# Performance work log

Hardware: AMD Instinct MI355X
Metric: run time of the kernel (lower is better)

## Reference

```python
import jax, jax.numpy as jnp
import numpy as np

N = 50000      # nodes
E = 800000     # edges
IN = 128       # in_channels
H = 128        # hidden_channels
OUT = 40       # out_channels (classes)
EPS = 1e-5     # LayerNorm eps


def _glorot(key, fan_in, fan_out):
    lim = np.sqrt(6.0 / (fan_in + fan_out)).astype(np.float32)
    return jax.random.uniform(key, (fan_in, fan_out), jnp.float32, -lim, lim)


def setup_inputs() -> dict:
    key = jax.random.key(0)
    ks = jax.random.split(key, 8)
    x = jax.random.normal(ks[0], (N, IN), jnp.float32)
    edge_index = jax.random.randint(ks[1], (2, E), 0, N, jnp.int32)
    return {
        "x": x,
        "W0": _glorot(ks[2], IN, H), "b0": jnp.zeros((H,), jnp.float32),
        "W1": _glorot(ks[3], H, H),  "b1": jnp.zeros((H,), jnp.float32),
        "W2": _glorot(ks[4], H, OUT), "b2": jnp.zeros((OUT,), jnp.float32),
        "ln1_g": jnp.ones((H,), jnp.float32), "ln1_b": jnp.zeros((H,), jnp.float32),
        "ln2_g": jnp.ones((H,), jnp.float32), "ln2_b": jnp.zeros((H,), jnp.float32),
        "edge_index": edge_index,
    }


def reference(x, W0, b0, W1, b1, W2, b2, ln1_g, ln1_b, ln2_g, ln2_b, edge_index):
    # GCN normalization with self-loops: A_hat = D^-1/2 (A + I) D^-1/2
    self_idx = jnp.arange(N, dtype=edge_index.dtype)
    src = jnp.concatenate([edge_index[0], self_idx])  # [E+N]
    dst = jnp.concatenate([edge_index[1], self_idx])
    deg = jax.ops.segment_sum(jnp.ones_like(src, jnp.float32), dst, num_segments=N)
    dinv = jax.lax.rsqrt(deg)  # deg >= 1 thanks to self-loops
    norm = dinv[src] * dinv[dst]  # [E+N]

    def conv(h, W, b):
        h = h @ W                                  # [N, F] dense GEMM
        msg = h[src] * norm[:, None]               # gather + scale [E+N, F]
        return jax.ops.segment_sum(msg, dst, num_segments=N) + b

    def layernorm(h, g, b):
        mu = jnp.mean(h, axis=-1, keepdims=True)
        var = jnp.mean(jnp.square(h - mu), axis=-1, keepdims=True)
        return (h - mu) * jax.lax.rsqrt(var + EPS) * g + b

    # layer 0 (note: original uses lns[i+1], so lns[0] is never applied)
    h = jax.nn.relu(layernorm(conv(x, W0, b0), ln1_g, ln1_b))
    # dropout is identity in eval mode
    h = jax.nn.relu(layernorm(conv(h, W1, b1), ln2_g, ln2_b))
    h = conv(h, W2, b2)
    return jax.nn.log_softmax(h, axis=-1)
```

## Files before the change

### kernel.cpp

```cpp
#include <hip/hip_runtime.h>
#include <math.h>

typedef __attribute__((ext_vector_type(8))) short bf16x8;
typedef __attribute__((ext_vector_type(4))) float f32x4;
typedef unsigned short u16;
typedef unsigned int u32;

static __device__ __forceinline__ u16 f2bf(float f) {
    unsigned u = __float_as_uint(f);
    unsigned r = (u + 0x7fff + ((u >> 16) & 1)) >> 16;
    return (u16)r;
}
static __device__ __forceinline__ float bf2f(u16 h) {
    return __uint_as_float(((unsigned)h) << 16);
}
static __device__ __forceinline__ float pk_lo(u32 u) { return __uint_as_float(u << 16); }
static __device__ __forceinline__ float pk_hi(u32 u) { return __uint_as_float(u & 0xffff0000u); }

__global__ void init_k(int* __restrict__ counts, int n, int gN,
                       const float* __restrict__ W0, const float* __restrict__ W1,
                       const float* __restrict__ W2,
                       u16* __restrict__ w0hi, u16* __restrict__ w0lo,
                       u16* __restrict__ w1hi, u16* __restrict__ w1lo,
                       u16* __restrict__ w2hi, u16* __restrict__ w2lo) {
    int b = blockIdx.x;
    if (b < gN) {
        int i = b * 256 + threadIdx.x;
        if (i < n) counts[i] = 0;
        return;
    }
    int i = (b - gN) * 256 + threadIdx.x;
    const float* W; u16 *hi, *lo; int COLS, cin, idx;
    if (i < 16384)      { W = W0; hi = w0hi; lo = w0lo; COLS = 128; cin = 128; idx = i; }
    else if (i < 32768) { W = W1; hi = w1hi; lo = w1lo; COLS = 128; cin = 128; idx = i - 16384; }
    else if (i < 40960) { W = W2; hi = w2hi; lo = w2lo; COLS = 64;  cin = 40;  idx = i - 32768; }
    else return;
    int k = idx / COLS, col = idx % COLS;
    float v = (col < cin) ? W[k * cin + col] : 0.f;
    u16 h = f2bf(v);
    u16 l = f2bf(v - bf2f(h));
    int ct = col >> 4, ks = k >> 5, ln = (col & 15) + (((k >> 3) & 3) << 4), j = k & 7;
    int pos = (((ct * 4 + ks) * 64 + ln) << 3) + j;
    hi[pos] = h; lo[pos] = l;
}

static __device__ __forceinline__ void gemm1_body(int bid, const float* __restrict__ A,
                                                  const u16* __restrict__ Whi,
                                                  const u16* __restrict__ Wlo,
                                                  u16* __restrict__ C, int nrows) {
    constexpr int COLS = 128;
    int wave = threadIdx.x >> 6, lane = threadIdx.x & 63;
    int r0 = bid * 64 + wave * 16;
    int arow = min(r0 + (lane & 15), nrows - 1);
    int kbase = (lane >> 4) * 8;

    bf16x8 ahi[4], alo[4];
#pragma unroll
    for (int ks = 0; ks < 4; ++ks) {
        const float* ap = &A[(long)arow * 128 + ks * 32 + kbase];
        float4 f0 = *(const float4*)ap;
        float4 f1 = *(const float4*)(ap + 4);
        float fv[8] = {f0.x, f0.y, f0.z, f0.w, f1.x, f1.y, f1.z, f1.w};
#pragma unroll
        for (int j = 0; j < 8; ++j) {
            u16 h = f2bf(fv[j]);
            ahi[ks][j] = (short)h;
            alo[ks][j] = (short)f2bf(fv[j] - bf2f(h));
        }
    }
#pragma unroll
    for (int ct = 0; ct < COLS / 16; ct += 2) {
        f32x4 acc0 = {0.f, 0.f, 0.f, 0.f}, acc1 = {0.f, 0.f, 0.f, 0.f};
#pragma unroll
        for (int ks = 0; ks < 4; ++ks) {
            int fo0 = ((ct * 4 + ks) * 64 + lane) * 8;
            int fo1 = (((ct + 1) * 4 + ks) * 64 + lane) * 8;
            bf16x8 bhi0 = *(const bf16x8*)&Whi[fo0];
            bf16x8 blo0 = *(const bf16x8*)&Wlo[fo0];
            bf16x8 bhi1 = *(const bf16x8*)&Whi[fo1];
            bf16x8 blo1 = *(const bf16x8*)&Wlo[fo1];
            acc0 = __builtin_amdgcn_mfma_f32_16x16x32_bf16(ahi[ks], bhi0, acc0, 0, 0, 0);
            acc1 = __builtin_amdgcn_mfma_f32_16x16x32_bf16(ahi[ks], bhi1, acc1, 0, 0, 0);
            acc0 = __builtin_amdgcn_mfma_f32_16x16x32_bf16(alo[ks], bhi0, acc0, 0, 0, 0);
            acc1 = __builtin_amdgcn_mfma_f32_16x16x32_bf16(alo[ks], bhi1, acc1, 0, 0, 0);
            acc0 = __builtin_amdgcn_mfma_f32_16x16x32_bf16(ahi[ks], blo0, acc0, 0, 0, 0);
            acc1 = __builtin_amdgcn_mfma_f32_16x16x32_bf16(ahi[ks], blo1, acc1, 0, 0, 0);
        }
#pragma unroll
        for (int r = 0; r < 4; ++r) {
            int orow = r0 + (lane >> 4) * 4 + r;
            if (orow < nrows) {
                C[(long)orow * COLS + ct * 16 + (lane & 15)] = f2bf(acc0[r]);
                C[(long)orow * COLS + (ct + 1) * 16 + (lane & 15)] = f2bf(acc1[r]);
            }
        }
    }
}

__global__ __launch_bounds__(256) void cg1_k(const int* __restrict__ dst,
                                             int* __restrict__ counts,
                                             u16* __restrict__ rank, int e,
                                             const float* __restrict__ A,
                                             const u16* __restrict__ Whi,
                                             const u16* __restrict__ Wlo,
                                             u16* __restrict__ C, int nrows, int gemmBlocks) {
    int bid = blockIdx.x;
    int k = bid / 5, r = bid % 5;
    if (r == 4) {
        if (k < gemmBlocks) gemm1_body(k, A, Whi, Wlo, C, nrows);
        return;
    }
    int i = (k * 4 + r) * 256 + threadIdx.x;
    if (i < e) rank[i] = (u16)atomicAdd(&counts[dst[i]], 1);
}

__global__ __launch_bounds__(1024) void scan1_k(const int* __restrict__ counts,
                                                int* __restrict__ offs,
                                                int* __restrict__ bsum,
                                                float* __restrict__ dinv, int n) {
    __shared__ int ws[16];
    int tid = threadIdx.x;
    int i = blockIdx.x * 1024 + tid;
    int lane = tid & 63, w = tid >> 6;
    int c = (i < n) ? counts[i] : 0;
    if (i < n) dinv[i] = rsqrtf((float)c + 1.0f);
    int s = c;
#pragma unroll
    for (int o = 1; o < 64; o <<= 1) { int t = __shfl_up(s, o); if (lane >= o) s += t; }
    if (lane == 63) ws[w] = s;
    __syncthreads();
    if (w == 0) {
        int x = (lane < 16) ? ws[lane] : 0;
#pragma unroll
        for (int o = 1; o < 16; o <<= 1) { int t = __shfl_up(x, o); if (lane >= o) x += t; }
        if (lane < 16) ws[lane] = x;
    }
    __syncthreads();
    int base = (w > 0) ? ws[w - 1] : 0;
    int incl = base + s;
    if (i < n) offs[i + 1] = incl;
    if (tid == 1023) bsum[blockIdx.x] = incl;
}
__global__ void scan23_k(int* __restrict__ offs, const int* __restrict__ bsum,
                         int nb, int n) {
    __shared__ int pre[64];
    int tid = threadIdx.x;
    if (tid < 64) {
        int v = (tid < nb) ? bsum[tid] : 0;
#pragma unroll
        for (int o = 1; o < 64; o <<= 1) { int t = __shfl_up(v, o); if (tid >= o) v += t; }
        pre[tid] = v;
    }
    __syncthreads();
    int i = blockIdx.x * 256 + tid;
    if (i == 0) offs[0] = 0;
    if (i < n) {
        int b = i >> 10;
        offs[i + 1] += (b > 0) ? pre[b - 1] : 0;
    }
}

__global__ __launch_bounds__(256) void fr_k(const int* __restrict__ src,
                                            const int* __restrict__ dst,
                                            const u16* __restrict__ rank,
                                            const int* __restrict__ offs,
                                            u16* __restrict__ csr, int e,
                                            u16* __restrict__ Cs,
                                            const float* __restrict__ dinv, int n) {
    int bid = blockIdx.x;
    int k = bid / 3, r = bid % 3;
    if (r == 2) {
        int i = k * 256 + threadIdx.x;
        if (i < e) csr[offs[dst[i]] + (int)rank[i]] = (u16)src[i];
        return;
    }
    int t = (k * 2 + r) * 256 + threadIdx.x;
    if (t >= n * 32) return;
    int row = t >> 5;
    float w = dinv[row];
    uint2 u = ((uint2*)Cs)[t];
    uint2 o2;
    o2.x = ((u32)f2bf(pk_hi(u.x) * w) << 16) | f2bf(pk_lo(u.x) * w);
    o2.y = ((u32)f2bf(pk_hi(u.y) * w) << 16) | f2bf(pk_lo(u.y) * w);
    ((uint2*)Cs)[t] = o2;
}

template<int COLS>
static __device__ __forceinline__ void gemm_body(int bid, const u16* __restrict__ A,
                                                 const u16* __restrict__ Whi,
                                                 const u16* __restrict__ Wlo,
                                                 const float* __restrict__ dinv,
                                                 u16* __restrict__ C, int rowOff, int rowEnd) {
    int wave = threadIdx.x >> 6, lane = threadIdx.x & 63;
    int r0 = rowOff + bid * 64 + wave * 16;
    if (r0 >= rowEnd) return;
    int arow = min(r0 + (lane & 15), rowEnd - 1);
    int kbase = (lane >> 4) * 8;

    bf16x8 a[4];
#pragma unroll
    for (int ks = 0; ks < 4; ++ks)
        a[ks] = *(const bf16x8*)&A[(long)arow * 128 + ks * 32 + kbase];

    float dscale[4];
#pragma unroll
    for (int r = 0; r < 4; ++r) {
        int orow = r0 + (lane >> 4) * 4 + r;
        dscale[r] = (orow < rowEnd) ? dinv[orow] : 0.f;
    }
#pragma unroll
    for (int ct = 0; ct < COLS / 16; ct += 2) {
        f32x4 acc0 = {0.f, 0.f, 0.f, 0.f}, acc1 = {0.f, 0.f, 0.f, 0.f};
#pragma unroll
        for (int ks = 0; ks < 4; ++ks) {
            int fo0 = ((ct * 4 + ks) * 64 + lane) * 8;
            int fo1 = (((ct + 1) * 4 + ks) * 64 + lane) * 8;
            bf16x8 bhi0 = *(const bf16x8*)&Whi[fo0];
            bf16x8 blo0 = *(const bf16x8*)&Wlo[fo0];
            bf16x8 bhi1 = *(const bf16x8*)&Whi[fo1];
            bf16x8 blo1 = *(const bf16x8*)&Wlo[fo1];
            acc0 = __builtin_amdgcn_mfma_f32_16x16x32_bf16(a[ks], bhi0, acc0, 0, 0, 0);
            acc1 = __builtin_amdgcn_mfma_f32_16x16x32_bf16(a[ks], bhi1, acc1, 0, 0, 0);
            acc0 = __builtin_amdgcn_mfma_f32_16x16x32_bf16(a[ks], blo0, acc0, 0, 0, 0);
            acc1 = __builtin_amdgcn_mfma_f32_16x16x32_bf16(a[ks], blo1, acc1, 0, 0, 0);
        }
#pragma unroll
        for (int r = 0; r < 4; ++r) {
            int orow = r0 + (lane >> 4) * 4 + r;
            if (orow < rowEnd) {
                C[(long)orow * COLS + ct * 16 + (lane & 15)] = f2bf(acc0[r] * dscale[r]);
                C[(long)orow * COLS + (ct + 1) * 16 + (lane & 15)] = f2bf(acc1[r] * dscale[r]);
            }
        }
    }
}

static __device__ __forceinline__ void agg_ln_body(int wid, int lane,
                                                   const u16* __restrict__ Cs,
                                                   const int* __restrict__ offs,
                                                   const u16* __restrict__ csr,
                                                   const float* __restrict__ dinv,
                                                   const float* __restrict__ bias,
                                                   const float* __restrict__ g,
                                                   const float* __restrict__ b,
                                                   u16* __restrict__ out) {
    const u32* C2 = (const u32*)Cs;
    u32 su = C2[(long)wid * 64 + lane];
    float ax = pk_lo(su), ay = pk_hi(su), bx2 = 0.f, by2 = 0.f;
    int beg = offs[wid], end = offs[wid + 1];
    int j = beg;
    while (j < end) {
        int take = min(64, end - j);
        int myidx = (lane < take) ? (int)csr[j + lane] : 0;
        int k = 0;
        for (; k + 8 <= take; k += 8) {
            int i0 = __shfl(myidx, k),     i1 = __shfl(myidx, k + 1);
            int i2 = __shfl(myidx, k + 2), i3 = __shfl(myidx, k + 3);
            int i4 = __shfl(myidx, k + 4), i5 = __shfl(myidx, k + 5);
            int i6 = __shfl(myidx, k + 6), i7 = __shfl(myidx, k + 7);
            u32 u0 = C2[(long)i0 * 64 + lane], u1 = C2[(long)i1 * 64 + lane];
            u32 u2 = C2[(long)i2 * 64 + lane], u3 = C2[(long)i3 * 64 + lane];
            u32 u4 = C2[(long)i4 * 64 + lane], u5 = C2[(long)i5 * 64 + lane];
            u32 u6 = C2[(long)i6 * 64 + lane], u7 = C2[(long)i7 * 64 + lane];
            ax += pk_lo(u0) + pk_lo(u1) + pk_lo(u2) + pk_lo(u3);
            ay += pk_hi(u0) + pk_hi(u1) + pk_hi(u2) + pk_hi(u3);
            bx2 += pk_lo(u4) + pk_lo(u5) + pk_lo(u6) + pk_lo(u7);
            by2 += pk_hi(u4) + pk_hi(u5) + pk_hi(u6) + pk_hi(u7);
        }
        for (; k < take; ++k) {
            int i0 = __shfl(myidx, k);
            u32 u0 = C2[(long)i0 * 64 + lane];
            ax += pk_lo(u0); ay += pk_hi(u0);
        }
        j += take;
    }
    float w = dinv[wid];
    float2 bia = ((const float2*)bias)[lane];
    float t0 = (ax + bx2) * w + bia.x;
    float t1 = (ay + by2) * w + bia.y;
    float s = t0 + t1;
#pragma unroll
    for (int off = 32; off; off >>= 1) s += __shfl_xor(s, off);
    float mu = s * (1.f / 128.f);
    float d0 = t0 - mu, d1 = t1 - mu;
    float v = d0 * d0 + d1 * d1;
#pragma unroll
    for (int off = 32; off; off >>= 1) v += __shfl_xor(v, off);
    float rstd = rsqrtf(v * (1.f / 128.f) + 1e-5f);
    float2 gv = ((const float2*)g)[lane];
    float2 bv = ((const float2*)b)[lane];
    float y0 = fmaxf(0.f, d0 * rstd * gv.x + bv.x);
    float y1 = fmaxf(0.f, d1 * rstd * gv.y + bv.y);
    ((u32*)out)[(long)wid * 64 + lane] = ((u32)f2bf(y1) << 16) | f2bf(y0);
}

__global__ __launch_bounds__(256) void agg_half_k(const u16* __restrict__ Cs,
                                                  const int* __restrict__ offs,
                                                  const u16* __restrict__ csr,
                                                  const float* __restrict__ dinv,
                                                  const float* __restrict__ bias,
                                                  const float* __restrict__ g,
                                                  const float* __restrict__ b,
                                                  u16* __restrict__ out,
                                                  int nodeOff, int nodeEnd) {
    int wid = nodeOff + ((blockIdx.x * 256 + threadIdx.x) >> 6);
    int lane = threadIdx.x & 63;
    if (wid >= nodeEnd) return;
    agg_ln_body(wid, lane, Cs, offs, csr, dinv, bias, g, b, out);
}

template<int COLS>
__global__ __launch_bounds__(256) void aggemm_k(const u16* __restrict__ CsAgg,
                                                const int* __restrict__ offs,
                                                const u16* __restrict__ csr,
                                                const float* __restrict__ dinv,
                                                const float* __restrict__ bias,
                                                const float* __restrict__ g,
                                                const float* __restrict__ b,
                                                u16* __restrict__ hOut,
                                                int nodeOff, int nodeEnd,
                                                const u16* __restrict__ A,
                                                const u16* __restrict__ Whi,
                                                const u16* __restrict__ Wlo,
                                                u16* __restrict__ C, int rowEnd, int gemmBlocks) {
    int bid = blockIdx.x;
    int k = bid / 17, r = bid % 17;
    if (r == 16) {
        if (k < gemmBlocks) gemm_body<COLS>(k, A, Whi, Wlo, dinv, C, 0, rowEnd);
        return;
    }
    int aggIdx = k * 16 + r;
    int wid = nodeOff + ((aggIdx * 256 + (int)threadIdx.x) >> 6);
    int lane = threadIdx.x & 63;
    if (wid >= nodeEnd) return;
    agg_ln_body(wid, lane, CsAgg, offs, csr, dinv, bias, g, b, hOut);
}

template<int COLS>
__global__ __launch_bounds__(256) void gemm_half_k(const u16* __restrict__ A,
                                                   const u16* __restrict__ Whi,
                                                   const u16* __restrict__ Wlo,
                                                   const float* __restrict__ dinv,
                                                   u16* __restrict__ C, int rowOff, int rowEnd) {
    gemm_body<COLS>(blockIdx.x, A, Whi, Wlo, dinv, C, rowOff, rowEnd);
}

__global__ __launch_bounds__(256) void agg_lsm_k(const u16* __restrict__ Cs,
                                                 const int* __restrict__ offs,
                                                 const u16* __restrict__ csr,
                                                 const float* __restrict__ dinv,
                                                 const float* __restrict__ b2,
                                                 float* __restrict__ out, int n) {
    int wid = (blockIdx.x * 256 + threadIdx.x) >> 6;
    int lane = threadIdx.x & 63;
    if (wid >= n) return;
    float aa = bf2f(Cs[(long)wid * 64 + lane]), ab = 0.f;
    int beg = offs[wid], end = offs[wid + 1];
    int j = beg;
    while (j < end) {
        int take = min(64, end - j);
        int myidx = (lane < take) ? (int)csr[j + lane] : 0;
        int k = 0;
        for (; k + 8 <= take; k += 8) {
            int i0 = __shfl(myidx, k),     i1 = __shfl(myidx, k + 1);
            int i2 = __shfl(myidx, k + 2), i3 = __shfl(myidx, k + 3);
            int i4 = __shfl(myidx, k + 4), i5 = __shfl(myidx, k + 5);
            int i6 = __shfl(myidx, k + 6), i7 = __shfl(myidx, k + 7);
            float v0 = bf2f(Cs[(long)i0 * 64 + lane]), v1 = bf2f(Cs[(long)i1 * 64 + lane]);
            float v2 = bf2f(Cs[(long)i2 * 64 + lane]), v3 = bf2f(Cs[(long)i3 * 64 + lane]);
            float v4 = bf2f(Cs[(long)i4 * 64 + lane]), v5 = bf2f(Cs[(long)i5 * 64 + lane]);
            float v6 = bf2f(Cs[(long)i6 * 64 + lane]), v7 = bf2f(Cs[(long)i7 * 64 + lane]);
            aa += v0 + v1 + v2 + v3;
            ab += v4 + v5 + v6 + v7;
        }
        for (; k < take; ++k) {
            int i0 = __shfl(myidx, k);
            aa += bf2f(Cs[(long)i0 * 64 + lane]);
        }
        j += take;
    }
    float v = (lane < 40) ? (aa + ab) * dinv[wid] + b2[lane] : -INFINITY;
    float m = v;
#pragma unroll
    for (int off = 32; off; off >>= 1) m = fmaxf(m, __shfl_xor(m, off));
    float e = (lane < 40) ? expf(v - m) : 0.f;
    float s = e;
#pragma unroll
    for (int off = 32; off; off >>= 1) s += __shfl_xor(s, off);
    float r = v - m - logf(s);
    if (lane < 40) out[(long)wid * 40 + lane] = r;
}

extern "C" void kernel_launch(void* const* d_in, const int* in_sizes, int n_in,
                              void* d_out, int out_size, void* d_ws, size_t ws_size,
                              hipStream_t stream) {
    const float* x    = (const float*)d_in[0];
    const float* W0   = (const float*)d_in[1];
    const float* b0   = (const float*)d_in[2];
    const float* W1   = (const float*)d_in[3];
    const float* b1   = (const float*)d_in[4];
    const float* W2   = (const float*)d_in[5];
    const float* b2   = (const float*)d_in[6];
    const float* ln1g = (const float*)d_in[7];
    const float* ln1b = (const float*)d_in[8];
    const float* ln2g = (const float*)d_in[9];
    const float* ln2b = (const float*)d_in[10];
    const int*   ei   = (const int*)d_in[11];

    const int N = in_sizes[0] / 128;
    const int E = in_sizes[11] / 2;
    const int* esrc = ei;
    const int* edst = ei + E;
    float* out = (float*)d_out;

    const int Npad = ((N + 255) / 256) * 256;
    const int N2 = N / 2;

    int* counts  = (int*)d_ws;
    int* offs    = counts + Npad;
    int* bsum    = offs + Npad;
    u16* rank16  = (u16*)(bsum + 64);
    u16* csr16   = rank16 + E;
    float* dinv  = (float*)(csr16 + E);
    u16* bufA    = (u16*)(dinv + Npad);
    u16* bufB    = bufA + (size_t)N * 128;
    u16* bufC    = bufB + (size_t)N * 128;
    u16* w0hi    = bufC + (size_t)N * 128;
    u16* w0lo    = w0hi + 16384;
    u16* w1hi    = w0lo + 16384;
    u16* w1lo    = w1hi + 16384;
    u16* w2hi    = w1lo + 16384;
    u16* w2lo    = w2hi + 8192;

    dim3 blk(256);
    int gN = (N + 255) / 256;
    int gE = (E + 255) / 256;
    int nb1024 = (N + 1023) / 1024;
    int gG = (N + 63) / 64;
    int gGh = (N2 + 63) / 64;
    int gAh = (N2 + 3) / 4;
    int gW = (N + 3) / 4;

    init_k<<<gN + 160, blk, 0, stream>>>(counts, N, gN, W0, W1, W2,
                                         w0hi, w0lo, w1hi, w1lo, w2hi, w2lo);
    cg1_k<<<5 * gG, blk, 0, stream>>>(edst, counts, rank16, E,
                                      x, w0hi, w0lo, bufA, N, gG);
    scan1_k<<<nb1024, 1024, 0, stream>>>(counts, offs, bsum, dinv, N);
    scan23_k<<<gN, blk, 0, stream>>>(offs, bsum, nb1024, N);
    fr_k<<<3 * gE, blk, 0, stream>>>(esrc, edst, rank16, offs, csr16, E, bufA, dinv, N);
    agg_half_k<<<gAh, blk, 0, stream>>>(bufA, offs, csr16, dinv, b0, ln1g, ln1b, bufB, 0, N2);
    aggemm_k<128><<<17 * gGh, blk, 0, stream>>>(bufA, offs, csr16, dinv, b0, ln1g, ln1b, bufB,
                                                N2, N, bufB, w1hi, w1lo, bufC, N2, gGh);
    gemm_half_k<128><<<gGh, blk, 0, stream>>>(bufB, w1hi, w1lo, dinv, bufC, N2, N);
    agg_half_k<<<gAh, blk, 0, stream>>>(bufC, offs, csr16, dinv, b1, ln2g, ln2b, bufA, 0, N2);
    aggemm_k<64><<<17 * gGh, blk, 0, stream>>>(bufC, offs, csr16, dinv, b1, ln2g, ln2b, bufA,
                                               N2, N, bufA, w2hi, w2lo, bufB, N2, gGh);
    gemm_half_k<64><<<gGh, blk, 0, stream>>>(bufA, w2hi, w2lo, dinv, bufB, N2, N);
    agg_lsm_k<<<gW, blk, 0, stream>>>(bufB, offs, csr16, dinv, b2, out, N);
}
```

Measured before the change: 205.7 us.

## Replace global atomic degree counting with per-block LDS histograms and partitioned scan

Degree counting no longer uses global atomics on a counts array. 256 blocks each build a shared-memory histogram of packed 16-bit counters, covering half the node range per pass, and store it to a slab. Three small kernels then form per-block exclusive prefixes, so the CSR fill can place edges deterministically. The first layer's source-side dinv prescale pass is removed: layer-0 aggregation multiplies each gathered neighbour row by dinv inside the gather loop, which adds extra scattered dinv loads. The design adds several kernel launches and assumes per-block counts fit in 16 bits.

```diff
diff --git a/kernel.cpp b/kernel.cpp
--- a/kernel.cpp
+++ b/kernel.cpp
@@ -17,19 +17,12 @@
 static __device__ __forceinline__ float pk_lo(u32 u) { return __uint_as_float(u << 16); }
 static __device__ __forceinline__ float pk_hi(u32 u) { return __uint_as_float(u & 0xffff0000u); }
 
-__global__ void init_k(int* __restrict__ counts, int n, int gN,
-                       const float* __restrict__ W0, const float* __restrict__ W1,
-                       const float* __restrict__ W2,
-                       u16* __restrict__ w0hi, u16* __restrict__ w0lo,
-                       u16* __restrict__ w1hi, u16* __restrict__ w1lo,
-                       u16* __restrict__ w2hi, u16* __restrict__ w2lo) {
-    int b = blockIdx.x;
-    if (b < gN) {
-        int i = b * 256 + threadIdx.x;
-        if (i < n) counts[i] = 0;
-        return;
-    }
-    int i = (b - gN) * 256 + threadIdx.x;
+__global__ void initw_k(const float* __restrict__ W0, const float* __restrict__ W1,
+                        const float* __restrict__ W2,
+                        u16* __restrict__ w0hi, u16* __restrict__ w0lo,
+                        u16* __restrict__ w1hi, u16* __restrict__ w1lo,
+                        u16* __restrict__ w2hi, u16* __restrict__ w2lo) {
+    int i = blockIdx.x * 256 + threadIdx.x;
     const float* W; u16 *hi, *lo; int COLS, cin, idx;
     if (i < 16384)      { W = W0; hi = w0hi; lo = w0lo; COLS = 128; cin = 128; idx = i; }
     else if (i < 32768) { W = W1; hi = w1hi; lo = w1lo; COLS = 128; cin = 128; idx = i - 16384; }
@@ -42,6 +35,119 @@
     int ct = col >> 4, ks = k >> 5, ln = (col & 15) + (((k >> 3) & 3) << 4), j = k & 7;
     int pos = (((ct * 4 + ks) * 64 + ln) << 3) + j;
     hi[pos] = h; lo[pos] = l;
+}
+
+__global__ __launch_bounds__(512) void hist_k(const int* __restrict__ dst,
+                                              u32* __restrict__ slab,
+                                              u16* __restrict__ rank,
+                                              int e, int epb, int nw) {
+    __shared__ u32 h[12544];
+    int b = blockIdx.x, tid = threadIdx.x;
+    int start = b * epb, end = min(e, start + epb);
+    int half_w = (nw + 1) / 2;
+    for (int half = 0; half < 2; ++half) {
+        int w0 = half * half_w;
+        int wn = min(half_w, nw - w0);
+        if (wn <= 0) break;
+        for (int w = tid; w < wn; w += 512) h[w] = 0;
+        __syncthreads();
+        for (int i = start + tid; i < end; i += 512) {
+            int d = dst[i];
+            int wd = d >> 1;
+            if (wd >= w0 && wd < w0 + wn) {
+                u32 sh = (u32)(d & 1) << 4;
+                u32 old = atomicAdd(&h[wd - w0], 1u << sh);
+                rank[i] = (u16)((old >> sh) & 0xffffu);
+            }
+        }
+        __syncthreads();
+        u32* row = slab + (size_t)b * nw + w0;
+        for (int w = tid; w < wn; w += 512) row[w] = h[w];
+        if (half == 0) __syncthreads();
+    }
+}
+
+__global__ void pscanA_k(const u32* __restrict__ slab, u32* __restrict__ gsum, int nw) {
+    int id = blockIdx.x * 256 + threadIdx.x;
+    if (id >= 16 * nw) return;
+    int g = id / nw, w = id - g * nw;
+    const u32* base = slab + (size_t)(g * 16) * nw + w;
+    u32 s = 0;
+#pragma unroll
+    for (int j = 0; j < 16; ++j) s += base[(size_t)j * nw];
+    gsum[(size_t)g * nw + w] = s;
+}
+__global__ void pscanB_k(u32* __restrict__ gsum, int* __restrict__ counts, int nw) {
+    int w = blockIdx.x * 256 + threadIdx.x;
+    if (w >= nw) return;
+    u32 run = 0;
+#pragma unroll
+    for (int g = 0; g < 16; ++g) {
+        u32 v = gsum[(size_t)g * nw + w];
+        gsum[(size_t)g * nw + w] = run;
+        run += v;
+    }
+    counts[2 * w] = (int)(run & 0xffffu);
+    counts[2 * w + 1] = (int)(run >> 16);
+}
+__global__ void pscanC_k(u32* __restrict__ slab, const u32* __restrict__ gsum, int nw) {
+    int id = blockIdx.x * 256 + threadIdx.x;
+    if (id >= 16 * nw) return;
+    int g = id / nw, w = id - g * nw;
+    u32 run = gsum[(size_t)g * nw + w];
+    u32* base = slab + (size_t)(g * 16) * nw + w;
+#pragma unroll
+    for (int j = 0; j < 16; ++j) {
+        u32 v = base[(size_t)j * nw];
+        base[(size_t)j * nw] = run;
+        run += v;
+    }
+}
+
+__global__ __launch_bounds__(1024) void scan1_k(const int* __restrict__ counts,
+                                                int* __restrict__ offs,
+                                                int* __restrict__ bsum,
+                                                float* __restrict__ dinv, int n) {
+    __shared__ int ws[16];
+    int tid = threadIdx.x;
+    int i = blockIdx.x * 1024 + tid;
+    int lane = tid & 63, w = tid >> 6;
+    int c = (i < n) ? counts[i] : 0;
+    if (i < n) dinv[i] = rsqrtf((float)c + 1.0f);
+    int s = c;
+#pragma unroll
+    for (int o = 1; o < 64; o <<= 1) { int t = __shfl_up(s, o); if (lane >= o) s += t; }
+    if (lane == 63) ws[w] = s;
+    __syncthreads();
+    if (w == 0) {
+        int x = (lane < 16) ? ws[lane] : 0;
+#pragma unroll
+        for (int o = 1; o < 16; o <<= 1) { int t = __shfl_up(x, o); if (lane >= o) x += t; }
+        if (lane < 16) ws[lane] = x;
+    }
+    __syncthreads();
+    int base = (w > 0) ? ws[w - 1] : 0;
+    int incl = base + s;
+    if (i < n) offs[i + 1] = incl;
+    if (tid == 1023) bsum[blockIdx.x] = incl;
+}
+__global__ void scan23_k(int* __restrict__ offs, const int* __restrict__ bsum,
+                         int nb, int n) {
+    __shared__ int pre[64];
+    int tid = threadIdx.x;
+    if (tid < 64) {
+        int v = (tid < nb) ? bsum[tid] : 0;
+#pragma unroll
+        for (int o = 1; o < 64; o <<= 1) { int t = __shfl_up(v, o); if (tid >= o) v += t; }
+        pre[tid] = v;
+    }
+    __syncthreads();
+    int i = blockIdx.x * 256 + tid;
+    if (i == 0) offs[0] = 0;
+    if (i < n) {
+        int b = i >> 10;
+        offs[i + 1] += (b > 0) ? pre[b - 1] : 0;
+    }
 }
 
 static __device__ __forceinline__ void gemm1_body(int bid, const float* __restrict__ A,
@@ -97,9 +203,13 @@
     }
 }
 
-__global__ __launch_bounds__(256) void cg1_k(const int* __restrict__ dst,
-                                             int* __restrict__ counts,
-                                             u16* __restrict__ rank, int e,
+__global__ __launch_bounds__(256) void fg1_k(const int* __restrict__ esrc,
+                                             const int* __restrict__ edst,
+                                             const u16* __restrict__ rank,
+                                             const int* __restrict__ offs,
+                                             const u32* __restrict__ slab,
+                                             u16* __restrict__ csr,
+                                             int e, int epb, int nw,
                                              const float* __restrict__ A,
                                              const u16* __restrict__ Whi,
                                              const u16* __restrict__ Wlo,
@@ -111,78 +221,13 @@
         return;
     }
     int i = (k * 4 + r) * 256 + threadIdx.x;
-    if (i < e) rank[i] = (u16)atomicAdd(&counts[dst[i]], 1);
-}
-
-__global__ __launch_bounds__(1024) void scan1_k(const int* __restrict__ counts,
-                                                int* __restrict__ offs,
-                                                int* __restrict__ bsum,
-                                                float* __restrict__ dinv, int n) {
-    __shared__ int ws[16];
-    int tid = threadIdx.x;
-    int i = blockIdx.x * 1024 + tid;
-    int lane = tid & 63, w = tid >> 6;
-    int c = (i < n) ? counts[i] : 0;
-    if (i < n) dinv[i] = rsqrtf((float)c + 1.0f);
-    int s = c;
-#pragma unroll
-    for (int o = 1; o < 64; o <<= 1) { int t = __shfl_up(s, o); if (lane >= o) s += t; }
-    if (lane == 63) ws[w] = s;
-    __syncthreads();
-    if (w == 0) {
-        int x = (lane < 16) ? ws[lane] : 0;
-#pragma unroll
-        for (int o = 1; o < 16; o <<= 1) { int t = __shfl_up(x, o); if (lane >= o) x += t; }
-        if (lane < 16) ws[lane] = x;
-    }
-    __syncthreads();
-    int base = (w > 0) ? ws[w - 1] : 0;
-    int incl = base + s;
-    if (i < n) offs[i + 1] = incl;
-    if (tid == 1023) bsum[blockIdx.x] = incl;
-}
-__global__ void scan23_k(int* __restrict__ offs, const int* __restrict__ bsum,
-                         int nb, int n) {
-    __shared__ int pre[64];
-    int tid = threadIdx.x;
-    if (tid < 64) {
-        int v = (tid < nb) ? bsum[tid] : 0;
-#pragma unroll
-        for (int o = 1; o < 64; o <<= 1) { int t = __shfl_up(v, o); if (tid >= o) v += t; }
-        pre[tid] = v;
-    }
-    __syncthreads();
-    int i = blockIdx.x * 256 + tid;
-    if (i == 0) offs[0] = 0;
-    if (i < n) {
-        int b = i >> 10;
-        offs[i + 1] += (b > 0) ? pre[b - 1] : 0;
-    }
-}
-
-__global__ __launch_bounds__(256) void fr_k(const int* __restrict__ src,
-                                            const int* __restrict__ dst,
-                                            const u16* __restrict__ rank,
-                                            const int* __restrict__ offs,
-                                            u16* __restrict__ csr, int e,
-                                            u16* __restrict__ Cs,
-                                            const float* __restrict__ dinv, int n) {
-    int bid = blockIdx.x;
-    int k = bid / 3, r = bid % 3;
-    if (r == 2) {
-        int i = k * 256 + threadIdx.x;
-        if (i < e) csr[offs[dst[i]] + (int)rank[i]] = (u16)src[i];
-        return;
-    }
-    int t = (k * 2 + r) * 256 + threadIdx.x;
-    if (t >= n * 32) return;
-    int row = t >> 5;
-    float w = dinv[row];
-    uint2 u = ((uint2*)Cs)[t];
-    uint2 o2;
-    o2.x = ((u32)f2bf(pk_hi(u.x) * w) << 16) | f2bf(pk_lo(u.x) * w);
-    o2.y = ((u32)f2bf(pk_hi(u.y) * w) << 16) | f2bf(pk_lo(u.y) * w);
-    ((uint2*)Cs)[t] = o2;
+    if (i < e) {
+        int d = edst[i];
+        int b = i / epb;
+        u32 word = slab[(size_t)b * nw + (d >> 1)];
+        int base = (int)((word >> ((u32)(d & 1) << 4)) & 0xffffu);
+        csr[offs[d] + base + (int)rank[i]] = (u16)esrc[i];
+    }
 }
 
 template<int COLS>
@@ -235,6 +280,7 @@
     }
 }
 
+template<bool PRESCALED>
 static __device__ __forceinline__ void agg_ln_body(int wid, int lane,
                                                    const u16* __restrict__ Cs,
                                                    const int* __restrict__ offs,
@@ -246,7 +292,8 @@
                                                    u16* __restrict__ out) {
     const u32* C2 = (const u32*)Cs;
     u32 su = C2[(long)wid * 64 + lane];
-    float ax = pk_lo(su), ay = pk_hi(su), bx2 = 0.f, by2 = 0.f;
+    float ss = PRESCALED ? 1.f : dinv[wid];
+    float ax = pk_lo(su) * ss, ay = pk_hi(su) * ss, bx2 = 0.f, by2 = 0.f;
     int beg = offs[wid], end = offs[wid + 1];
     int j = beg;
     while (j < end) {
@@ -254,23 +301,30 @@
         int myidx = (lane < take) ? (int)csr[j + lane] : 0;
         int k = 0;
         for (; k + 8 <= take; k += 8) {
-            int i0 = __shfl(myidx, k),     i1 = __shfl(myidx, k + 1);
-            int i2 = __shfl(myidx, k + 2), i3 = __shfl(myidx, k + 3);
-            int i4 = __shfl(myidx, k + 4), i5 = __shfl(myidx, k + 5);
-            int i6 = __shfl(myidx, k + 6), i7 = __shfl(myidx, k + 7);
-            u32 u0 = C2[(long)i0 * 64 + lane], u1 = C2[(long)i1 * 64 + lane];
-            u32 u2 = C2[(long)i2 * 64 + lane], u3 = C2[(long)i3 * 64 + lane];
-            u32 u4 = C2[(long)i4 * 64 + lane], u5 = C2[(long)i5 * 64 + lane];
-            u32 u6 = C2[(long)i6 * 64 + lane], u7 = C2[(long)i7 * 64 + lane];
-            ax += pk_lo(u0) + pk_lo(u1) + pk_lo(u2) + pk_lo(u3);
-            ay += pk_hi(u0) + pk_hi(u1) + pk_hi(u2) + pk_hi(u3);
-            bx2 += pk_lo(u4) + pk_lo(u5) + pk_lo(u6) + pk_lo(u7);
-            by2 += pk_hi(u4) + pk_hi(u5) + pk_hi(u6) + pk_hi(u7);
+            int is[8];
+#pragma unroll
+            for (int q = 0; q < 8; ++q) is[q] = __shfl(myidx, k + q);
+            float ds[8];
+            if (!PRESCALED) {
+#pragma unroll
+                for (int q = 0; q < 8; ++q) ds[q] = dinv[is[q]];
+            }
+            u32 us[8];
+#pragma unroll
+            for (int q = 0; q < 8; ++q) us[q] = C2[(long)is[q] * 64 + lane];
+#pragma unroll
+            for (int q = 0; q < 8; ++q) {
+                float f0 = pk_lo(us[q]), f1 = pk_hi(us[q]);
+                if (!PRESCALED) { f0 *= ds[q]; f1 *= ds[q]; }
+                if (q < 4) { ax += f0; ay += f1; }
+                else       { bx2 += f0; by2 += f1; }
+            }
         }
         for (; k < take; ++k) {
             int i0 = __shfl(myidx, k);
+            float dv = PRESCALED ? 1.f : dinv[i0];
             u32 u0 = C2[(long)i0 * 64 + lane];
-            ax += pk_lo(u0); ay += pk_hi(u0);
+            ax += pk_lo(u0) * dv; ay += pk_hi(u0) * dv;
         }
         j += take;
     }
@@ -294,6 +348,7 @@
     ((u32*)out)[(long)wid * 64 + lane] = ((u32)f2bf(y1) << 16) | f2bf(y0);
 }
 
+template<bool PRESCALED>
 __global__ __launch_bounds__(256) void agg_half_k(const u16* __restrict__ Cs,
                                                   const int* __restrict__ offs,
                                                   const u16* __restrict__ csr,
@@ -306,10 +361,10 @@
     int wid = nodeOff + ((blockIdx.x * 256 + threadIdx.x) >> 6);
     int lane = threadIdx.x & 63;
     if (wid >= nodeEnd) return;
-    agg_ln_body(wid, lane, Cs, offs, csr, dinv, bias, g, b, out);
-}
-
-template<int COLS>
+    agg_ln_body<PRESCALED>(wid, lane, Cs, offs, csr, dinv, bias, g, b, out);
+}
+
+template<int COLS, bool PRESCALED>
 __global__ __launch_bounds__(256) void aggemm_k(const u16* __restrict__ CsAgg,
                                                 const int* __restrict__ offs,
                                                 const u16* __restrict__ csr,
@@ -333,7 +388,7 @@
     int wid = nodeOff + ((aggIdx * 256 + (int)threadIdx.x) >> 6);
     int lane = threadIdx.x & 63;
     if (wid >= nodeEnd) return;
-    agg_ln_body(wid, lane, CsAgg, offs, csr, dinv, bias, g, b, hOut);
+    agg_ln_body<PRESCALED>(wid, lane, CsAgg, offs, csr, dinv, bias, g, b, hOut);
 }
 
 template<int COLS>
@@ -415,6 +470,8 @@
 
     const int Npad = ((N + 255) / 256) * 256;
     const int N2 = N / 2;
+    const int NW = (N + 1) / 2;
+    const int EPB = (E + 255) / 256;
 
     int* counts  = (int*)d_ws;
     int* offs    = counts + Npad;
@@ -431,30 +488,35 @@
     u16* w1lo    = w1hi + 16384;
     u16* w2hi    = w1lo + 16384;
     u16* w2lo    = w2hi + 8192;
+    u32* gsum    = (u32*)(w2lo + 8192);
+    u32* slab    = (u32*)bufB;
 
     dim3 blk(256);
     int gN = (N + 255) / 256;
-    int gE = (E + 255) / 256;
     int nb1024 = (N + 1023) / 1024;
     int gG = (N + 63) / 64;
     int gGh = (N2 + 63) / 64;
     int gAh = (N2 + 3) / 4;
     int gW = (N + 3) / 4;
-
-    init_k<<<gN + 160, blk, 0, stream>>>(counts, N, gN, W0, W1, W2,
-                                         w0hi, w0lo, w1hi, w1lo, w2hi, w2lo);
-    cg1_k<<<5 * gG, blk, 0, stream>>>(edst, counts, rank16, E,
-                                      x, w0hi, w0lo, bufA, N, gG);
+    int gA16 = (16 * NW + 255) / 256;
+    int gB1 = (NW + 255) / 256;
+
+    initw_k<<<160, blk, 0, stream>>>(W0, W1, W2, w0hi, w0lo, w1hi, w1lo, w2hi, w2lo);
+    hist_k<<<256, 512, 0, stream>>>(edst, slab, rank16, E, EPB, NW);
+    pscanA_k<<<gA16, blk, 0, stream>>>(slab, gsum, NW);
+    pscanB_k<<<gB1, blk, 0, stream>>>(gsum, counts, NW);
+    pscanC_k<<<gA16, blk, 0, stream>>>(slab, gsum, NW);
     scan1_k<<<nb1024, 1024, 0, stream>>>(counts, offs, bsum, dinv, N);
     scan23_k<<<gN, blk, 0, stream>>>(offs, bsum, nb1024, N);
-    fr_k<<<3 * gE, blk, 0, stream>>>(esrc, edst, rank16, offs, csr16, E, bufA, dinv, N);
-    agg_half_k<<<gAh, blk, 0, stream>>>(bufA, offs, csr16, dinv, b0, ln1g, ln1b, bufB, 0, N2);
-    aggemm_k<128><<<17 * gGh, blk, 0, stream>>>(bufA, offs, csr16, dinv, b0, ln1g, ln1b, bufB,
-                                                N2, N, bufB, w1hi, w1lo, bufC, N2, gGh);
+    fg1_k<<<5 * gG, blk, 0, stream>>>(esrc, edst, rank16, offs, slab, csr16, E, EPB, NW,
+                                      x, w0hi, w0lo, bufA, N, gG);
+    agg_half_k<false><<<gAh, blk, 0, stream>>>(bufA, offs, csr16, dinv, b0, ln1g, ln1b, bufB, 0, N2);
+    aggemm_k<128, false><<<17 * gGh, blk, 0, stream>>>(bufA, offs, csr16, dinv, b0, ln1g, ln1b, bufB,
+                                                       N2, N, bufB, w1hi, w1lo, bufC, N2, gGh);
     gemm_half_k<128><<<gGh, blk, 0, stream>>>(bufB, w1hi, w1lo, dinv, bufC, N2, N);
-    agg_half_k<<<gAh, blk, 0, stream>>>(bufC, offs, csr16, dinv, b1, ln2g, ln2b, bufA, 0, N2);
-    aggemm_k<64><<<17 * gGh, blk, 0, stream>>>(bufC, offs, csr16, dinv, b1, ln2g, ln2b, bufA,
-                                               N2, N, bufA, w2hi, w2lo, bufB, N2, gGh);
+    agg_half_k<true><<<gAh, blk, 0, stream>>>(bufC, offs, csr16, dinv, b1, ln2g, ln2b, bufA, 0, N2);
+    aggemm_k<64, true><<<17 * gGh, blk, 0, stream>>>(bufC, offs, csr16, dinv, b1, ln2g, ln2b, bufA,
+                                                     N2, N, bufA, w2hi, w2lo, bufB, N2, gGh);
     gemm_half_k<64><<<gGh, blk, 0, stream>>>(bufA, w2hi, w2lo, dinv, bufB, N2, N);
     agg_lsm_k<<<gW, blk, 0, stream>>>(bufB, offs, csr16, dinv, b2, out, N);
 }
```

Measured after the change: 210.8 us. 1.02x slower.
